# Kernel optimization log

Hardware: AMD Instinct MI355X
Metric: run time of the kernel (lower is better)

The kernel has to match this reference:

```python
import jax, jax.numpy as jnp
import numpy as np


def setup_inputs() -> dict:
    key = jax.random.key(0)
    k0, k1, k2, k3 = jax.random.split(key, 4)
    T, B, K, L, DEG = 2000, 2048, 64, 64, 3
    return {
        "currents": jax.random.normal(k0, (T, B), dtype=jnp.float32),
        "a": jax.random.normal(k1, (K,), dtype=jnp.float32) * 0.05,
        "b_lag": jax.random.normal(k2, (L,), dtype=jnp.float32) * 1e-3,
        "poly_coeff": jax.random.normal(k3, (1, DEG + 1), dtype=jnp.float32) * 0.3,
        "b_act": jnp.zeros((1,), dtype=jnp.float32),
        "max_current": jnp.full((1,), 100.0, dtype=jnp.float32),
        "max_firing_rate": jnp.full((1,), 100.0, dtype=jnp.float32),
    }


def _poly_act(z, poly_coeff, b_act, max_current, max_firing_rate):
    # PolynomialActivation.forward: x=(z-b)/max_current; poly=sum_d x^d * coeff_d^2
    x = (z - b_act[0]) / max_current[0]  # [B]
    deg = poly_coeff.shape[1] - 1
    coeff = (poly_coeff ** 2)[0]  # [deg+1]
    # build integer powers safely (negative bases) via repeated multiply
    pows = [jnp.ones_like(x)]
    for _ in range(deg):
        pows.append(pows[-1] * x)
    powers = jnp.stack(pows, axis=-1)  # [B, deg+1]
    poly = powers @ coeff  # [B]
    return jax.nn.relu(max_firing_rate[0] * jnp.tanh(poly))


def reference(currents, a, b_lag, poly_coeff, b_act, max_current, max_firing_rate):
    T, B = currents.shape
    K, L = a.shape[0], b_lag.shape[0]

    def step(carry, c_t):
        cur_buf, fs_buf = carry  # [B,K], [B,L]
        cur_buf = jnp.concatenate([cur_buf[:, 1:], c_t[:, None]], axis=1)
        x = cur_buf @ a                      # einsum('j,ij->i')
        y = 1000.0 * (fs_buf @ b_lag)        # einsum('j,ij->i')
        f = _poly_act(x + y, poly_coeff, b_act, max_current, max_firing_rate)
        fs_buf = jnp.concatenate([fs_buf[:, 1:], f[:, None]], axis=1)
        return (cur_buf, fs_buf), f

    init = (jnp.zeros((B, K), currents.dtype), jnp.zeros((B, L), currents.dtype))
    _, fs = jax.lax.scan(step, init, currents)  # fs: [T, B]
    return fs
```

## Files before the change

kernel.cpp:

```cpp
#include <hip/hip_runtime.h>

#define T_STEPS 2000
#define BATCH   2048

#define FORCE_VGPR(x) asm("" : "+v"(x))

__global__ __launch_bounds__(256) void fused_kernel(
    const float* __restrict__ currents, const float* __restrict__ a,
    const float* __restrict__ b_lag, const float* __restrict__ poly_coeff,
    const float* __restrict__ b_act, const float* __restrict__ max_current,
    const float* __restrict__ max_firing_rate, float* __restrict__ out)
{
    int tid  = threadIdx.x;
    int lane = tid & 63;
    int wid  = tid >> 6;
    int b    = blockIdx.x * 4 + wid;

    float inv = 1.0f / max_current[0];
    float cba = -b_act[0] * inv;
    float af  = a[63 - lane] * inv;
    float gam = (1000.0f * inv) * b_lag[63 - lane];

    const float K2 = 2.8853900817779268f;
    float c0 = poly_coeff[0], c1 = poly_coeff[1], c2 = poly_coeff[2], c3 = poly_coeff[3];
    float k0 = K2 * c0 * c0, k1 = K2 * c1 * c1, k2 = K2 * c2 * c2, k3 = K2 * c3 * c3;
    float M  = max_firing_rate[0];
    float m2 = -2.0f * M;

    FORCE_VGPR(cba); FORCE_VGPR(af); FORCE_VGPR(gam);
    FORCE_VGPR(k0);  FORCE_VGPR(k1); FORCE_VGPR(k2); FORCE_VGPR(k3);
    FORCE_VGPR(M);   FORCE_VGPR(m2);

    auto bcast = [](float v, int l) {
        return __builtin_bit_cast(float,
            __builtin_amdgcn_readlane(__builtin_bit_cast(int, v), l));
    };
    auto rotl1 = [](float v) {
        int i = __builtin_bit_cast(int, v);
        return __builtin_bit_cast(float,
            __builtin_amdgcn_update_dpp(i, i, 0x134, 0xf, 0xf, false));
    };

    const float* ccol   = currents + b;
    float*       outcol = out + b;

    bool  is63 = (lane == 63);
    float R  = cba;
    float cv = ccol[(long)lane * BATCH];
    float F  = 0.0f;

    auto step = [&](int s) {
        float c = bcast(cv, s);
        R = fmaf(af, c, R);
        float u = bcast(R, 0);
        FORCE_VGPR(u);
        float u2 = u * u;
        float a1 = fmaf(u, k1, k0);
        float a2 = fmaf(u, k3, k2);
        float p  = fmaf(u2, a2, a1);
        float e  = __builtin_amdgcn_exp2f(p);
        float r  = __builtin_amdgcn_rcpf(e + 1.0f);
        float f  = fmaxf(fmaf(m2, r, M), 0.0f);
        float Rr = rotl1(R);
        Rr = is63 ? cba : Rr;
        R  = fmaf(gam, f, Rr);
        float Fr = rotl1(F);
        F  = is63 ? f : Fr;
        (void)s;
    };

    for (int chunk = 0; chunk < 31; ++chunk) {
        int t0 = chunk * 64;
        int tp = t0 + 64 + lane;
        float cv_next = (tp < T_STEPS) ? ccol[(long)tp * BATCH] : 0.0f;
#pragma unroll
        for (int s = 0; s < 64; ++s) step(s);
        outcol[(long)(t0 + lane) * BATCH] = F;
        cv = cv_next;
    }
#pragma unroll
    for (int s = 0; s < 16; ++s) step(s);
    if (lane >= 48) outcol[(long)(1984 + lane - 48) * BATCH] = F;
}

extern "C" void kernel_launch(void* const* d_in, const int* in_sizes, int n_in,
                              void* d_out, int out_size, void* d_ws, size_t ws_size,
                              hipStream_t stream) {
    const float* currents   = (const float*)d_in[0];
    const float* a          = (const float*)d_in[1];
    const float* b_lag      = (const float*)d_in[2];
    const float* poly_coeff = (const float*)d_in[3];
    const float* b_act      = (const float*)d_in[4];
    const float* mc         = (const float*)d_in[5];
    const float* mfr        = (const float*)d_in[6];
    float* out = (float*)d_out;

    fused_kernel<<<BATCH / 4, 256, 0, stream>>>(
        currents, a, b_lag, poly_coeff, b_act, mc, mfr, out);
}
```

Baseline: 219.9 us.

## Replace exp/rcp tanh with clamped rational approximation and scalar current loads

The exp2-plus-reciprocal tanh evaluation is replaced by a clamped Padé-style rational polynomial that needs a single reciprocal, and the polynomial is rewritten in Horner form. Currents are now loaded through a wave-uniform pointer, so each step reads a scalar instead of doing a readlane broadcast from a VGPR. The VGPR-forcing asm hints are removed. This aims to shorten the serial per-step dependency chain, at the cost of a tanh approximation whose accuracy depends on the clamp range, and of 64 scalar loads per chunk that are no longer prefetched one chunk ahead.

After: 263.7 us. +19.9%, slower.

```diff
diff --git a/kernel.cpp b/kernel.cpp
--- a/kernel.cpp
+++ b/kernel.cpp
@@ -2,8 +2,6 @@
 
 #define T_STEPS 2000
 #define BATCH   2048
-
-#define FORCE_VGPR(x) asm("" : "+v"(x))
 
 __global__ __launch_bounds__(256) void fused_kernel(
     const float* __restrict__ currents, const float* __restrict__ a,
@@ -21,66 +19,65 @@
     float af  = a[63 - lane] * inv;
     float gam = (1000.0f * inv) * b_lag[63 - lane];
 
-    const float K2 = 2.8853900817779268f;
     float c0 = poly_coeff[0], c1 = poly_coeff[1], c2 = poly_coeff[2], c3 = poly_coeff[3];
-    float k0 = K2 * c0 * c0, k1 = K2 * c1 * c1, k2 = K2 * c2 * c2, k3 = K2 * c3 * c3;
+    float k0 = c0 * c0, k1 = c1 * c1, k2 = c2 * c2, k3 = c3 * c3;
     float M  = max_firing_rate[0];
-    float m2 = -2.0f * M;
+    float N0 = 135135.0f * M, N1 = 17325.0f * M, N2 = 378.0f * M;
+    const float D0 = 135135.0f, D1 = 62370.0f, D2 = 3150.0f, D3 = 28.0f;
 
-    FORCE_VGPR(cba); FORCE_VGPR(af); FORCE_VGPR(gam);
-    FORCE_VGPR(k0);  FORCE_VGPR(k1); FORCE_VGPR(k2); FORCE_VGPR(k3);
-    FORCE_VGPR(M);   FORCE_VGPR(m2);
-
-    auto bcast = [](float v, int l) {
-        return __builtin_bit_cast(float,
-            __builtin_amdgcn_readlane(__builtin_bit_cast(int, v), l));
-    };
     auto rotl1 = [](float v) {
         int i = __builtin_bit_cast(int, v);
         return __builtin_bit_cast(float,
             __builtin_amdgcn_update_dpp(i, i, 0x134, 0xf, 0xf, false));
     };
 
-    const float* ccol   = currents + b;
-    float*       outcol = out + b;
+    const float* ccol = currents + b;
+    uint64_t pv  = (uint64_t)(uintptr_t)ccol;
+    uint32_t plo = (uint32_t)__builtin_amdgcn_readfirstlane((int)(pv & 0xffffffffu));
+    uint32_t phi = (uint32_t)__builtin_amdgcn_readfirstlane((int)(pv >> 32));
+    const float* cc = (const float*)(uintptr_t)(((uint64_t)phi << 32) | plo);
+
+    float* outcol = out + b;
 
     bool  is63 = (lane == 63);
-    float R  = cba;
-    float cv = ccol[(long)lane * BATCH];
-    float F  = 0.0f;
+    float R = cba;
+    float F = 0.0f;
 
-    auto step = [&](int s) {
-        float c = bcast(cv, s);
+    auto step = [&](float c) {
         R = fmaf(af, c, R);
-        float u = bcast(R, 0);
-        FORCE_VGPR(u);
-        float u2 = u * u;
-        float a1 = fmaf(u, k1, k0);
-        float a2 = fmaf(u, k3, k2);
-        float p  = fmaf(u2, a2, a1);
-        float e  = __builtin_amdgcn_exp2f(p);
-        float r  = __builtin_amdgcn_rcpf(e + 1.0f);
-        float f  = fmaxf(fmaf(m2, r, M), 0.0f);
+        float u = __builtin_bit_cast(float,
+                    __builtin_amdgcn_readlane(__builtin_bit_cast(int, R), 0));
+        float p = fmaf(fmaf(fmaf(k3, u, k2), u, k1), u, k0);
+        float q = __builtin_amdgcn_fmed3f(p, 0.0f, 5.0f);
+        float w = q * q;
+        float N = fmaf(w, fmaf(w, fmaf(w, M,  N2), N1), N0);
+        float D = fmaf(w, fmaf(w, fmaf(w, D3, D2), D1), D0);
+        float r = __builtin_amdgcn_rcpf(D);
+        float f = (q * N) * r;
         float Rr = rotl1(R);
         Rr = is63 ? cba : Rr;
         R  = fmaf(gam, f, Rr);
         float Fr = rotl1(F);
         F  = is63 ? f : Fr;
-        (void)s;
     };
 
     for (int chunk = 0; chunk < 31; ++chunk) {
-        int t0 = chunk * 64;
-        int tp = t0 + 64 + lane;
-        float cv_next = (tp < T_STEPS) ? ccol[(long)tp * BATCH] : 0.0f;
+        long t0 = (long)chunk * 64;
+        float cs[64];
 #pragma unroll
-        for (int s = 0; s < 64; ++s) step(s);
-        outcol[(long)(t0 + lane) * BATCH] = F;
-        cv = cv_next;
+        for (int s = 0; s < 64; ++s) cs[s] = cc[(t0 + s) * BATCH];
+#pragma unroll
+        for (int s = 0; s < 64; ++s) step(cs[s]);
+        outcol[(t0 + lane) * BATCH] = F;
     }
+    {
+        float cs[16];
 #pragma unroll
-    for (int s = 0; s < 16; ++s) step(s);
-    if (lane >= 48) outcol[(long)(1984 + lane - 48) * BATCH] = F;
+        for (int s = 0; s < 16; ++s) cs[s] = cc[(long)(1984 + s) * BATCH];
+#pragma unroll
+        for (int s = 0; s < 16; ++s) step(cs[s]);
+        if (lane >= 48) outcol[(long)(1984 + lane - 48) * BATCH] = F;
+    }
 }
 
 extern "C" void kernel_launch(void* const* d_in, const int* in_sizes, int n_in,
```
